# Performance work log

Hardware: AMD Instinct MI355X
Metric: run time of the kernel (lower is better)

The kernel has to match this reference:

```python
import jax, jax.numpy as jnp
import numpy as np

N_TOKENS = 8192
D_IN = 4096
D_OUT = 4096
N_EXPERTS = 8
LORA_R = 16
LORA_ALPHA = 32.0
SCALING = LORA_ALPHA / LORA_R
MAX_THRESHOLD = 1.0 / N_EXPERTS


def setup_inputs() -> dict:
    key = jax.random.key(0)
    ks = jax.random.split(key, 7)
    s_in = 1.0 / np.sqrt(D_IN)
    s_r = 1.0 / np.sqrt(LORA_R)
    return {
        "inputs": jax.random.normal(ks[0], (N_TOKENS, D_IN), jnp.float32),
        "router_w": jax.random.uniform(ks[1], (N_EXPERTS, D_IN), jnp.float32, -s_in, s_in),
        "router_b": jax.random.uniform(ks[2], (N_EXPERTS,), jnp.float32, -s_in, s_in),
        "thr_w": jax.random.uniform(ks[3], (1, D_IN), jnp.float32, -s_in, s_in),
        "thr_b": jax.random.uniform(ks[4], (1,), jnp.float32, -s_in, s_in),
        # lora_A per expert: [E, r, D_IN]; lora_B per expert: [E, D_OUT, r]
        # (original inits lora_B to zeros; randomized here for a meaningful baseline)
        "lora_A": jax.random.uniform(ks[5], (N_EXPERTS, LORA_R, D_IN), jnp.float32, -s_in, s_in),
        "lora_B": jax.random.uniform(ks[6], (N_EXPERTS, D_OUT, LORA_R), jnp.float32, -s_r, s_r),
    }


def reference(inputs, router_w, router_b, thr_w, thr_b, lora_A, lora_B):
    # gating
    logits = inputs @ router_w.T + router_b                      # [N, E]
    gate = jax.nn.softmax(logits, axis=-1)                       # [N, E]
    thr = jax.nn.sigmoid(inputs @ thr_w.T + thr_b) * MAX_THRESHOLD  # [N, 1]
    adapted = gate - thr                                         # [N, E]
    selected = (adapted >= 0).astype(inputs.dtype)               # [N, E]
    weights = adapted * selected                                 # [N, E]
    wsum = jnp.sum(weights, axis=-1, keepdims=True)
    wsum = jnp.where(wsum == 0, jnp.ones_like(wsum), wsum)
    weights = weights / wsum                                     # [N, E]
    # experts: LoRA, linear so masked-weight 0 == not running the expert
    h = jnp.einsum('nd,erd->ner', inputs, lora_A)                # [N, E, r]
    wh = h * weights[:, :, None]                                 # [N, E, r] (tiny)
    results = jnp.einsum('ner,eor->no', wh, lora_B) * SCALING    # [N, D_OUT]
    return results
```

## Files before the change

kernel.cpp:

```cpp
#include <hip/hip_runtime.h>
#include <stdint.h>


typedef __bf16 bf16x8 __attribute__((ext_vector_type(8)));
typedef float f32x4 __attribute__((ext_vector_type(4)));
typedef __attribute__((address_space(1))) const void* gp_t;
typedef __attribute__((address_space(3))) void* lp_t;

__device__ __forceinline__ f32x4 mfma16(bf16x8 a, bf16x8 b, f32x4 c) {
  return __builtin_amdgcn_mfma_f32_16x16x32_bf16(a, b, c, 0, 0, 0);
}
__device__ __forceinline__ uint32_t bfbits(float f) {
  uint32_t u = __builtin_bit_cast(uint32_t, f);
  return (u + 0x7fffu + ((u >> 16) & 1u)) >> 16;
}
__device__ __forceinline__ uint32_t pk2(float a, float b) {
  return bfbits(a) | (bfbits(b) << 16);
}

#define LDS_BARRIER() do {                                   \
    asm volatile("s_waitcnt lgkmcnt(0)" ::: "memory");       \
    __builtin_amdgcn_sched_barrier(0);                       \
    __builtin_amdgcn_s_barrier();                            \
    __builtin_amdgcn_sched_barrier(0);                       \
  } while (0)

__global__ void pack_all(const float* __restrict__ rw, const float* __restrict__ tw,
                         const float* __restrict__ la, const float* __restrict__ lb,
                         uint4* __restrict__ W1p, uint4* __restrict__ B2p) {
  if (blockIdx.x < 288) {
    int id = blockIdx.x * 256 + threadIdx.x;
    int lane = id & 63, k32 = (id >> 6) & 127, ct = id >> 13;
    int row = ct * 16 + (lane & 15);
    int col = k32 * 32 + (lane >> 4) * 8;
    const float* src = nullptr;
    if (row < 128)      src = la + (size_t)row * 4096 + col;
    else if (row < 136) src = rw + (size_t)(row - 128) * 4096 + col;
    else if (row == 136) src = tw + col;
    float v[8];
#pragma unroll
    for (int j = 0; j < 8; ++j) v[j] = src ? src[j] : 0.f;
    uint4 u;
    u.x = pk2(v[0], v[1]); u.y = pk2(v[2], v[3]);
    u.z = pk2(v[4], v[5]); u.w = pk2(v[6], v[7]);
    W1p[(size_t)(ct * 128 + k32) * 64 + lane] = u;
  } else {
    int id = (blockIdx.x - 288) * 256 + threadIdx.x;
    int lane = id & 63, ks = (id >> 6) & 3, ct = id >> 8;
    int o = ct * 16 + (lane & 15);
    int k0 = ks * 32 + (lane >> 4) * 8;
    const float* s = lb + (size_t)(k0 >> 4) * 65536 + (size_t)o * 16 + (k0 & 15);
    uint4 u;
    u.x = pk2(s[0] * 2.f, s[1] * 2.f); u.y = pk2(s[2] * 2.f, s[3] * 2.f);
    u.z = pk2(s[4] * 2.f, s[5] * 2.f); u.w = pk2(s[6] * 2.f, s[7] * 2.f);
    B2p[(size_t)(ct * 4 + ks) * 64 + lane] = u;
  }
}

__global__ __launch_bounds__(1024) void k1_gate(
    const float* __restrict__ inp, const uint4* __restrict__ W1p,
    const float* __restrict__ rb, const float* __restrict__ tb,
    unsigned short* __restrict__ wh) {
  __shared__ __align__(16) char smem[76800];
  char* const Ab  = smem;
  char* const whl = smem + 65536;
  float* const scores = (float*)(smem + 73728);
  float* const wgt    = (float*)(smem + 75776);

  const int t = threadIdx.x;
  const int lane = t & 63;
  const int w = t >> 6;
  const int kg = w >> 3;
  const int ct_ = w & 7;
  const int l15 = lane & 15;
  const int lq = lane >> 4;
  const int n0 = blockIdx.x * 32;
  const int rx = (l15 & 7) << 4;

  const int srow = t >> 5;
  const int scf = t & 31;
  const float* ap = inp + (size_t)(n0 + srow) * 4096 + scf * 4;
  const int sx = (srow & 7) << 4;

  f32x4 accO[2] = {}, acc8[2] = {};
  float4 av[2][4];

  const uint4* wown = W1p + (size_t)(ct_ * 128) * 64 + lane;
  const uint4* w8b  = W1p + (size_t)(8 * 128) * 64 + lane;

#pragma unroll
  for (int g = 0; g < 2; ++g)
#pragma unroll
    for (int j = 0; j < 4; ++j)
      av[g][j] = *(const float4*)(ap + (size_t)(g * 4) * 512 + j * 128);
#pragma unroll
  for (int g = 0; g < 2; ++g) {
    char* d2 = Ab + g * 32768 + srow * 1024;
#pragma unroll
    for (int j = 0; j < 4; ++j) {
      uint2 u; u.x = pk2(av[g][j].x, av[g][j].y); u.y = pk2(av[g][j].z, av[g][j].w);
      *(uint2*)(d2 + ((scf * 8 + j * 256) ^ sx)) = u;
    }
  }
  LDS_BARRIER();

  for (int c = 0; c < 4; ++c) {
    if (c < 3) {
#pragma unroll
      for (int g = 0; g < 2; ++g)
#pragma unroll
        for (int j = 0; j < 4; ++j)
          av[g][j] = *(const float4*)(ap + (size_t)(g * 4 + c + 1) * 512 + j * 128);
    }
    const int ck = kg * 4 + c;
    const char* A0 = Ab + kg * 32768;
#pragma unroll
    for (int ks = 0; ks < 16; ++ks) {
      bf16x8 b = __builtin_bit_cast(bf16x8, wown[(size_t)(ck * 16 + ks) * 64]);
      bf16x8 a0 = *(const bf16x8*)(A0 + l15 * 1024 + ((ks * 64 + lq * 16) ^ rx));
      bf16x8 a1 = *(const bf16x8*)(A0 + (16 + l15) * 1024 + ((ks * 64 + lq * 16) ^ rx));
      accO[0] = mfma16(a0, b, accO[0]);
      accO[1] = mfma16(a1, b, accO[1]);
    }
#pragma unroll
    for (int ii = 0; ii < 2; ++ii) {
      const int ks8 = ct_ + ii * 8;
      bf16x8 b8 = __builtin_bit_cast(bf16x8, w8b[(size_t)(ck * 16 + ks8) * 64]);
      bf16x8 a0 = *(const bf16x8*)(A0 + l15 * 1024 + ((ks8 * 64 + lq * 16) ^ rx));
      bf16x8 a1 = *(const bf16x8*)(A0 + (16 + l15) * 1024 + ((ks8 * 64 + lq * 16) ^ rx));
      acc8[0] = mfma16(a0, b8, acc8[0]);
      acc8[1] = mfma16(a1, b8, acc8[1]);
    }
    if (c < 3) {
      LDS_BARRIER();
#pragma unroll
      for (int g = 0; g < 2; ++g) {
        char* d2 = Ab + g * 32768 + srow * 1024;
#pragma unroll
        for (int j = 0; j < 4; ++j) {
          uint2 u; u.x = pk2(av[g][j].x, av[g][j].y); u.y = pk2(av[g][j].z, av[g][j].w);
          *(uint2*)(d2 + ((scf * 8 + j * 256) ^ sx)) = u;
        }
      }
    }
    LDS_BARRIER();
  }

  *(f32x4*)(Ab + (size_t)((w * 2 + 0) * 64 + lane) * 16) = accO[0];
  *(f32x4*)(Ab + (size_t)((w * 2 + 1) * 64 + lane) * 16) = accO[1];
  *(f32x4*)(Ab + 32768 + (size_t)((w * 2 + 0) * 64 + lane) * 16) = acc8[0];
  *(f32x4*)(Ab + 32768 + (size_t)((w * 2 + 1) * 64 + lane) * 16) = acc8[1];
  LDS_BARRIER();
  f32x4 hO[2] = {};
  if (w < 8) {
#pragma unroll
    for (int tt = 0; tt < 2; ++tt) {
      f32x4 x = *(const f32x4*)(Ab + (size_t)((w * 2 + tt) * 64 + lane) * 16);
      f32x4 y = *(const f32x4*)(Ab + (size_t)(((w + 8) * 2 + tt) * 64 + lane) * 16);
#pragma unroll
      for (int r_ = 0; r_ < 4; ++r_) hO[tt][r_] = x[r_] + y[r_];
    }
  }
  if (t < 512) {
    const int tok = t >> 4, col = t & 15;
    const int tt = tok >> 4, lq_ = (tok >> 2) & 3, r_ = tok & 3;
    float sv = 0.f;
#pragma unroll
    for (int w2 = 0; w2 < 16; ++w2)
      sv += *(const float*)(Ab + 32768 +
            (size_t)((w2 * 2 + tt) * 64 + lq_ * 16 + col) * 16 + r_ * 4);
    scores[tok * 16 + col] = sv;
  }
  LDS_BARRIER();
  if (t < 32) {
    float l_[9];
#pragma unroll
    for (int e = 0; e < 9; ++e) l_[e] = scores[t * 16 + e];
    float mx = -3.4e38f;
#pragma unroll
    for (int e = 0; e < 8; ++e) { l_[e] += rb[e]; mx = fmaxf(mx, l_[e]); }
    float g[8], s = 0.f;
#pragma unroll
    for (int e = 0; e < 8; ++e) { g[e] = __expf(l_[e] - mx); s += g[e]; }
    const float thr = 0.125f / (1.f + __expf(-(l_[8] + tb[0])));
    const float inv = 1.f / s;
    float wv[8], ws = 0.f;
#pragma unroll
    for (int e = 0; e < 8; ++e) { wv[e] = fmaxf(g[e] * inv - thr, 0.f); ws += wv[e]; }
    const float wn = (ws == 0.f) ? 1.f : ws;
#pragma unroll
    for (int e = 0; e < 8; ++e) wgt[t * 8 + e] = wv[e] / wn;
  }
  LDS_BARRIER();
  if (w < 8) {
#pragma unroll
    for (int tt = 0; tt < 2; ++tt)
#pragma unroll
      for (int r_ = 0; r_ < 4; ++r_) {
        const int tok = tt * 16 + lq * 4 + r_;
        *(unsigned short*)(whl + tok * 256 + (((w * 16 + l15) * 2) ^ ((tok & 7) << 4))) =
            (unsigned short)bfbits(hO[tt][r_] * wgt[tok * 8 + w]);
      }
  }
  LDS_BARRIER();
  if (t < 512) {
    const int row = t >> 4, seg = t & 15;
    ((uint4*)(wh + (size_t)(n0 + row) * 128))[seg] =
        ((const uint4*)(whl + row * 256))[seg];
  }
}

__global__ __launch_bounds__(512, 4) void k2_out(
    const unsigned short* __restrict__ wh, const uint4* __restrict__ B2p,
    float* __restrict__ out) {
  __shared__ __align__(16) char Bl[32768];
  __shared__ __align__(16) char Ob[32768];
  const int t = threadIdx.x, lane = t & 63, w = t >> 6;
  const int l15 = lane & 15, lq = lane >> 4;
  const int bid = blockIdx.x;
  const int tokg = bid >> 5, colg = bid & 31;
  const int n0 = tokg * 256, c0 = colg * 128;

  {
    const uint4* src = B2p + (size_t)(colg * 32) * 64;
#pragma unroll
    for (int i = 0; i < 4; ++i)
      __builtin_amdgcn_global_load_lds((gp_t)(const void*)(src + i * 512 + t),
          (lp_t)(void*)(Bl + (i * 512 + w * 64) * 16), 16, 0, 0);
  }
  __syncthreads();

  const int srow = t >> 3, sseg = t & 7;
  const int swz = (srow & 7) << 4;

#pragma unroll
  for (int tt = 0; tt < 2; ++tt) {
    const int tok = n0 + tt * 128 + w * 16 + l15;
    bf16x8 pa[4];
    const uint4* whu = (const uint4*)wh + (size_t)tok * 16;
#pragma unroll
    for (int ks = 0; ks < 4; ++ks)
      pa[ks] = __builtin_bit_cast(bf16x8, whu[(ks * 4 + lq) ^ (l15 & 7)]);
    f32x4 acc[8] = {};
#pragma unroll
    for (int ct = 0; ct < 8; ++ct)
#pragma unroll
      for (int ks = 0; ks < 4; ++ks) {
        bf16x8 b = *(const bf16x8*)(Bl + (size_t)((ct * 4 + ks) * 64 + lane) * 16);
        acc[ct] = mfma16(b, pa[ks], acc[ct]);
      }
#pragma unroll
    for (int sr = 0; sr < 2; ++sr) {
      if ((w >> 2) == sr) {
        const int tl = (w & 3) * 16 + l15;
        char* d = Ob + tl * 512;
#pragma unroll
        for (int ct = 0; ct < 8; ++ct)
          *(f32x4*)(d + ((ct * 64 + lq * 16) ^ ((tl & 7) << 4))) = acc[ct];
      }
      LDS_BARRIER();
      {
        float* op = out + (size_t)(n0 + tt * 128 + sr * 64 + srow) * 4096 + c0 + sseg * 4;
#pragma unroll
        for (int j = 0; j < 4; ++j) {
          f32x4 v = *(const f32x4*)(Ob + srow * 512 + ((sseg * 16 + j * 128) ^ swz));
          __builtin_nontemporal_store(v, (f32x4*)(op + j * 32));
        }
      }
      LDS_BARRIER();
    }
  }
}

extern "C" void kernel_launch(void* const* d_in, const int* in_sizes, int n_in,
                              void* d_out, int out_size, void* d_ws, size_t ws_size,
                              hipStream_t stream) {
  (void)in_sizes; (void)n_in; (void)out_size; (void)ws_size;
  const float* inp      = (const float*)d_in[0];
  const float* router_w = (const float*)d_in[1];
  const float* router_b = (const float*)d_in[2];
  const float* thr_w    = (const float*)d_in[3];
  const float* thr_b    = (const float*)d_in[4];
  const float* lora_A   = (const float*)d_in[5];
  const float* lora_B   = (const float*)d_in[6];
  float* out = (float*)d_out;

  char* ws = (char*)d_ws;
  uint4*          W1p = (uint4*)ws;
  uint4*          B2p = (uint4*)(ws + 1179648);
  unsigned short* wh  = (unsigned short*)(ws + 1179648 + 1048576);

  pack_all<<<544, 256, 0, stream>>>(router_w, thr_w, lora_A, lora_B, W1p, B2p);
  k1_gate<<<256, 1024, 0, stream>>>(inp, W1p, router_b, thr_b, wh);
  k2_out<<<1024, 512, 0, stream>>>(wh, B2p, out);
}
```

Measured before the change: 67.00 us.

## Split k1_gate across two blocks per token tile by expert half

k1_gate now launches two blocks per 32-token tile, each computing the LoRA-A projection for half of the experts (4 of 8 column tiles), with the 16 waves split 4 ways along K instead of 2 ways. This doubles the grid to fill more CUs and cuts per-block MFMA work. In exchange, each input tile is read and converted to bf16 twice, and the router/threshold scores are recomputed redundantly in both blocks.

```diff
diff --git a/kernel.cpp b/kernel.cpp
--- a/kernel.cpp
+++ b/kernel.cpp
@@ -61,20 +61,23 @@
     const float* __restrict__ inp, const uint4* __restrict__ W1p,
     const float* __restrict__ rb, const float* __restrict__ tb,
     unsigned short* __restrict__ wh) {
-  __shared__ __align__(16) char smem[76800];
+  __shared__ __align__(16) char smem[72704];
   char* const Ab  = smem;
   char* const whl = smem + 65536;
-  float* const scores = (float*)(smem + 73728);
-  float* const wgt    = (float*)(smem + 75776);
+  float* const scores = (float*)(smem + 69632);
+  float* const wgt    = (float*)(smem + 71680);
 
   const int t = threadIdx.x;
   const int lane = t & 63;
   const int w = t >> 6;
-  const int kg = w >> 3;
-  const int ct_ = w & 7;
+  const int t_ = w & 3;
+  const int q  = w >> 2;
   const int l15 = lane & 15;
   const int lq = lane >> 4;
-  const int n0 = blockIdx.x * 32;
+  const int tokg = blockIdx.x >> 1;
+  const int half = blockIdx.x & 1;
+  const int n0 = tokg * 32;
+  const int ct_ = half * 4 + t_;
   const int rx = (l15 & 7) << 4;
 
   const int srow = t >> 5;
@@ -83,23 +86,26 @@
   const int sx = (srow & 7) << 4;
 
   f32x4 accO[2] = {}, acc8[2] = {};
-  float4 av[2][4];
+  float4 avA[4], avB[4];
 
   const uint4* wown = W1p + (size_t)(ct_ * 128) * 64 + lane;
   const uint4* w8b  = W1p + (size_t)(8 * 128) * 64 + lane;
 
 #pragma unroll
-  for (int g = 0; g < 2; ++g)
-#pragma unroll
-    for (int j = 0; j < 4; ++j)
-      av[g][j] = *(const float4*)(ap + (size_t)(g * 4) * 512 + j * 128);
-#pragma unroll
-  for (int g = 0; g < 2; ++g) {
-    char* d2 = Ab + g * 32768 + srow * 1024;
+  for (int j = 0; j < 4; ++j) avA[j] = *(const float4*)(ap + j * 128);
+#pragma unroll
+  for (int j = 0; j < 4; ++j) avB[j] = *(const float4*)(ap + (j + 4) * 128);
+  {
+    char* d2 = Ab + srow * 2048;
 #pragma unroll
     for (int j = 0; j < 4; ++j) {
-      uint2 u; u.x = pk2(av[g][j].x, av[g][j].y); u.y = pk2(av[g][j].z, av[g][j].w);
+      uint2 u; u.x = pk2(avA[j].x, avA[j].y); u.y = pk2(avA[j].z, avA[j].w);
       *(uint2*)(d2 + ((scf * 8 + j * 256) ^ sx)) = u;
+    }
+#pragma unroll
+    for (int j = 0; j < 4; ++j) {
+      uint2 u; u.x = pk2(avB[j].x, avB[j].y); u.y = pk2(avB[j].z, avB[j].w);
+      *(uint2*)(d2 + ((scf * 8 + (j + 4) * 256) ^ sx)) = u;
     }
   }
   LDS_BARRIER();
@@ -107,40 +113,44 @@
   for (int c = 0; c < 4; ++c) {
     if (c < 3) {
 #pragma unroll
-      for (int g = 0; g < 2; ++g)
-#pragma unroll
-        for (int j = 0; j < 4; ++j)
-          av[g][j] = *(const float4*)(ap + (size_t)(g * 4 + c + 1) * 512 + j * 128);
-    }
-    const int ck = kg * 4 + c;
-    const char* A0 = Ab + kg * 32768;
-#pragma unroll
-    for (int ks = 0; ks < 16; ++ks) {
-      bf16x8 b = __builtin_bit_cast(bf16x8, wown[(size_t)(ck * 16 + ks) * 64]);
-      bf16x8 a0 = *(const bf16x8*)(A0 + l15 * 1024 + ((ks * 64 + lq * 16) ^ rx));
-      bf16x8 a1 = *(const bf16x8*)(A0 + (16 + l15) * 1024 + ((ks * 64 + lq * 16) ^ rx));
+      for (int j = 0; j < 4; ++j)
+        avA[j] = *(const float4*)(ap + (size_t)(c + 1) * 1024 + j * 128);
+    }
+#pragma unroll
+    for (int s = 0; s < 8; ++s) {
+      const int kl = s * 4 + q;
+      bf16x8 b = __builtin_bit_cast(bf16x8, wown[(size_t)(c * 32 + kl) * 64]);
+      bf16x8 a0 = *(const bf16x8*)(Ab + l15 * 2048 + ((kl * 64 + lq * 16) ^ rx));
+      bf16x8 a1 = *(const bf16x8*)(Ab + (16 + l15) * 2048 + ((kl * 64 + lq * 16) ^ rx));
       accO[0] = mfma16(a0, b, accO[0]);
       accO[1] = mfma16(a1, b, accO[1]);
     }
-#pragma unroll
-    for (int ii = 0; ii < 2; ++ii) {
-      const int ks8 = ct_ + ii * 8;
-      bf16x8 b8 = __builtin_bit_cast(bf16x8, w8b[(size_t)(ck * 16 + ks8) * 64]);
-      bf16x8 a0 = *(const bf16x8*)(A0 + l15 * 1024 + ((ks8 * 64 + lq * 16) ^ rx));
-      bf16x8 a1 = *(const bf16x8*)(A0 + (16 + l15) * 1024 + ((ks8 * 64 + lq * 16) ^ rx));
+    if (c < 3) {
+#pragma unroll
+      for (int j = 0; j < 4; ++j)
+        avB[j] = *(const float4*)(ap + (size_t)(c + 1) * 1024 + (j + 4) * 128);
+    }
+#pragma unroll
+    for (int i = 0; i < 2; ++i) {
+      const int ks8 = (2 * t_ + i) * 4 + q;
+      bf16x8 b8 = __builtin_bit_cast(bf16x8, w8b[(size_t)(c * 32 + ks8) * 64]);
+      bf16x8 a0 = *(const bf16x8*)(Ab + l15 * 2048 + ((ks8 * 64 + lq * 16) ^ rx));
+      bf16x8 a1 = *(const bf16x8*)(Ab + (16 + l15) * 2048 + ((ks8 * 64 + lq * 16) ^ rx));
       acc8[0] = mfma16(a0, b8, acc8[0]);
       acc8[1] = mfma16(a1, b8, acc8[1]);
     }
     if (c < 3) {
       LDS_BARRIER();
-#pragma unroll
-      for (int g = 0; g < 2; ++g) {
-        char* d2 = Ab + g * 32768 + srow * 1024;
-#pragma unroll
-        for (int j = 0; j < 4; ++j) {
-          uint2 u; u.x = pk2(av[g][j].x, av[g][j].y); u.y = pk2(av[g][j].z, av[g][j].w);
-          *(uint2*)(d2 + ((scf * 8 + j * 256) ^ sx)) = u;
-        }
+      char* d2 = Ab + srow * 2048;
+#pragma unroll
+      for (int j = 0; j < 4; ++j) {
+        uint2 u; u.x = pk2(avA[j].x, avA[j].y); u.y = pk2(avA[j].z, avA[j].w);
+        *(uint2*)(d2 + ((scf * 8 + j * 256) ^ sx)) = u;
+      }
+#pragma unroll
+      for (int j = 0; j < 4; ++j) {
+        uint2 u; u.x = pk2(avB[j].x, avB[j].y); u.y = pk2(avB[j].z, avB[j].w);
+        *(uint2*)(d2 + ((scf * 8 + (j + 4) * 256) ^ sx)) = u;
       }
     }
     LDS_BARRIER();
@@ -152,13 +162,15 @@
   *(f32x4*)(Ab + 32768 + (size_t)((w * 2 + 1) * 64 + lane) * 16) = acc8[1];
   LDS_BARRIER();
   f32x4 hO[2] = {};
-  if (w < 8) {
+  if (w < 4) {
 #pragma unroll
     for (int tt = 0; tt < 2; ++tt) {
-      f32x4 x = *(const f32x4*)(Ab + (size_t)((w * 2 + tt) * 64 + lane) * 16);
-      f32x4 y = *(const f32x4*)(Ab + (size_t)(((w + 8) * 2 + tt) * 64 + lane) * 16);
-#pragma unroll
-      for (int r_ = 0; r_ < 4; ++r_) hO[tt][r_] = x[r_] + y[r_];
+#pragma unroll
+      for (int qq = 0; qq < 4; ++qq) {
+        f32x4 x = *(const f32x4*)(Ab + (size_t)(((w + 4 * qq) * 2 + tt) * 64 + lane) * 16);
+#pragma unroll
+        for (int r_ = 0; r_ < 4; ++r_) hO[tt][r_] += x[r_];
+      }
     }
   }
   if (t < 512) {
@@ -192,21 +204,21 @@
     for (int e = 0; e < 8; ++e) wgt[t * 8 + e] = wv[e] / wn;
   }
   LDS_BARRIER();
-  if (w < 8) {
+  if (w < 4) {
 #pragma unroll
     for (int tt = 0; tt < 2; ++tt)
 #pragma unroll
       for (int r_ = 0; r_ < 4; ++r_) {
         const int tok = tt * 16 + lq * 4 + r_;
-        *(unsigned short*)(whl + tok * 256 + (((w * 16 + l15) * 2) ^ ((tok & 7) << 4))) =
-            (unsigned short)bfbits(hO[tt][r_] * wgt[tok * 8 + w]);
-      }
-  }
-  LDS_BARRIER();
-  if (t < 512) {
-    const int row = t >> 4, seg = t & 15;
-    ((uint4*)(wh + (size_t)(n0 + row) * 128))[seg] =
-        ((const uint4*)(whl + row * 256))[seg];
+        *(unsigned short*)(whl + tok * 128 + (((w * 16 + l15) * 2) ^ ((tok & 7) << 4))) =
+            (unsigned short)bfbits(hO[tt][r_] * wgt[tok * 8 + half * 4 + w]);
+      }
+  }
+  LDS_BARRIER();
+  if (t < 256) {
+    const int row = t >> 3, seg = t & 7;
+    ((uint4*)(wh + (size_t)(n0 + row) * 128 + half * 64))[seg] =
+        ((const uint4*)(whl + row * 128))[seg];
   }
 }
 
@@ -291,6 +303,6 @@
   unsigned short* wh  = (unsigned short*)(ws + 1179648 + 1048576);
 
   pack_all<<<544, 256, 0, stream>>>(router_w, thr_w, lora_A, lora_B, W1p, B2p);
-  k1_gate<<<256, 1024, 0, stream>>>(inp, W1p, router_b, thr_b, wh);
+  k1_gate<<<512, 1024, 0, stream>>>(inp, W1p, router_b, thr_b, wh);
   k2_out<<<1024, 512, 0, stream>>>(wh, B2p, out);
 }
```

Measured after the change: 103.1 us. 1.54x slower.
